# Performance work log

Hardware: AMD Instinct MI355X
Metric: run time of the kernel (lower is better)

## Reference

```python
import jax, jax.numpy as jnp
import numpy as np

# dims per init_kwargs / input_specs
B, S, HID = 4, 2048, 1024
H = 16          # num_heads
DH = HID // H   # head_dim = 64
G = 1024        # group_size; grouped feature dim = S*DH//G = 128
SCALE = 1.0 / (DH ** 0.5)


def setup_inputs() -> dict:
    key = jax.random.key(0)
    ks = jax.random.split(key, 9)
    w = lambda k: jax.random.normal(k, (HID, HID), jnp.float32) * 0.02
    b = lambda k: jax.random.normal(k, (HID,), jnp.float32) * 0.02
    return {
        "hidden_states": jax.random.normal(ks[0], (B, S, HID), jnp.float32),
        "Wq": w(ks[1]), "bq": b(ks[2]),
        "Wk": w(ks[3]), "bk": b(ks[4]),
        "Wv": w(ks[5]), "bv": b(ks[6]),
        "Wo": w(ks[7]), "bo": b(ks[8]),
    }


def reference(hidden_states, Wq, bq, Wk, bk, Wv, bv, Wo, bo):
    Bs, Ss, _ = hidden_states.shape

    def proj(W, bias):
        # torch nn.Linear: x @ W.T + b
        y = hidden_states @ W.T + bias                      # [B,S,HID]
        y = y.reshape(Bs, Ss, H, DH).transpose(0, 2, 1, 3)  # [B,H,S,DH]
        # grouped view: fold seq/head_dim into G groups of S*DH//G features
        return y.reshape(Bs, H, G, -1)                      # [B,H,G,S*DH/G]

    q, k, v = proj(Wq, bq), proj(Wk, bk), proj(Wv, bv)
    scores = jnp.einsum("bhgd,bhkd->bhgk", q, k) * SCALE    # [B,H,G,G]
    probs = jax.nn.softmax(scores, axis=-1)                 # dropout: eval mode (identity)
    ctx = jnp.einsum("bhgk,bhkd->bhgd", probs, v)           # [B,H,G,S*DH/G]
    ctx = ctx.transpose(0, 2, 1, 3).reshape(Bs, -1, HID)    # [B,S,HID]
    return ctx @ Wo.T + bo
```

## Files before the change

### kernel.cpp

```cpp
#include <hip/hip_runtime.h>


typedef __attribute__((ext_vector_type(8))) short short8;
typedef __attribute__((ext_vector_type(4))) float f32x4;
typedef unsigned int u32;
typedef unsigned short u16;

#define MFMA16(a, b, c) __builtin_amdgcn_mfma_f32_16x16x32_bf16((a), (b), (c), 0, 0, 0)

union S8 { short8 s; uint2 v[2]; u32 u[4]; };

__device__ __forceinline__ u32 f2bf1(float x) {
    union { float f; u32 u; } v; v.f = x;
    return (v.u + 0x7fffu + ((v.u >> 16) & 1u)) >> 16;
}

__device__ __forceinline__ u32 cvtpk(float lo, float hi) {
    u32 r;
    asm("v_cvt_pk_bf16_f32 %0, %1, %2" : "=v"(r) : "v"(lo), "v"(hi));
    return r;
}

__device__ __forceinline__ void gld16(u16* lds, const u16* g) {
    __builtin_amdgcn_global_load_lds(
        (const __attribute__((address_space(1))) unsigned int*)(g),
        (__attribute__((address_space(3))) unsigned int*)(lds),
        16, 0, 0);
}

__global__ __launch_bounds__(256) void convert(
    const float* __restrict__ X, const float* __restrict__ Wq,
    const float* __restrict__ Wk, const float* __restrict__ Wv,
    const float* __restrict__ Wo,
    u16* __restrict__ Xb, u16* __restrict__ Wcat, u16* __restrict__ Wob)
{
    const size_t M8 = 8388608, M1 = 1048576;
    size_t i = ((size_t)blockIdx.x * 256 + threadIdx.x) * 16;
    const float* src; u16* dst;
    if (i < M8)              { src = X  + i;                dst = Xb   + i; }
    else if (i < M8 + M1)    { src = Wq + (i - M8);         dst = Wcat + (i - M8); }
    else if (i < M8 + 2*M1)  { src = Wk + (i - M8 - M1);    dst = Wcat + (i - M8); }
    else if (i < M8 + 3*M1)  { src = Wv + (i - M8 - 2*M1);  dst = Wcat + (i - M8); }
    else                     { src = Wo + (i - M8 - 3*M1);  dst = Wob  + (i - M8 - 3*M1); }
#pragma unroll
    for (int j = 0; j < 2; ++j) {
        float4 a = ((const float4*)src)[2 * j];
        float4 b = ((const float4*)src)[2 * j + 1];
        uint4 o;
        o.x = f2bf1(a.x) | (f2bf1(a.y) << 16);
        o.y = f2bf1(a.z) | (f2bf1(a.w) << 16);
        o.z = f2bf1(b.x) | (f2bf1(b.y) << 16);
        o.w = f2bf1(b.z) | (f2bf1(b.w) << 16);
        ((uint4*)dst)[j] = o;
    }
}

__global__ __launch_bounds__(256, 2) void qkv_gemm10(
    const u16* __restrict__ Xb, const u16* __restrict__ Wcat,
    const float* __restrict__ b0, const float* __restrict__ b1,
    const float* __restrict__ b2,
    u16* __restrict__ q_att, u16* __restrict__ k_att, u16* __restrict__ v_t)
{
    const int nb = blockIdx.x, mb = blockIdx.y;
    const int mat = nb >> 3;

    __shared__ __align__(16) u16 As[2][128 * 64];
    __shared__ __align__(16) u16 Bs[2][128 * 64];

    const int t = threadIdx.x, wave = t >> 6, lane = t & 63;
    const int l15 = lane & 15, quad = lane >> 4;
    const int wm = (wave >> 1) * 64, wn = (wave & 1) * 64;

    const int srow = t >> 3;
    const int scol = ((t & 7) ^ (srow & 7)) * 8;

    const u16* Ab = Xb   + (size_t)(mb * 128) * 1024;
    const u16* Bb = Wcat + (size_t)(nb * 128) * 1024;

    const int swz = l15 & 7;

#define QSTAGE(pp, k0_) do {                                                  \
        _Pragma("unroll")                                                     \
        for (int c_ = 0; c_ < 4; ++c_) {                                      \
            size_t so_ = (size_t)(c_ * 32 + srow) * 1024 + (k0_) + scol;      \
            gld16(&As[(pp)][wave * 512 + c_ * 2048], Ab + so_);               \
            gld16(&Bs[(pp)][wave * 512 + c_ * 2048], Bb + so_);               \
        }                                                                     \
    } while (0)

    f32x4 acc[4][4] = {};

    QSTAGE(0, 0);
    __syncthreads();

    for (int kt = 0; kt < 16; ++kt) {
        const int p = kt & 1;
        if (kt + 1 < 16) QSTAGE(p ^ 1, (kt + 1) * 64);
        const u16* Asp = &As[p][0];
        const u16* Bsp = &Bs[p][0];

#pragma unroll
        for (int ks = 0; ks < 2; ++ks) {
            short8 af[4], bf[4];
            const int ck = ((ks * 4 + quad) ^ swz) * 8;
#pragma unroll
            for (int mt = 0; mt < 4; ++mt)
                af[mt] = *(const short8*)(Asp + (wm + mt * 16 + l15) * 64 + ck);
#pragma unroll
            for (int nt = 0; nt < 4; ++nt)
                bf[nt] = *(const short8*)(Bsp + (wn + nt * 16 + l15) * 64 + ck);
#pragma unroll
            for (int mt = 0; mt < 4; ++mt)
#pragma unroll
                for (int nt = 0; nt < 4; ++nt)
                    acc[mt][nt] = MFMA16(af[mt], bf[nt], acc[mt][nt]);
        }

        if (kt + 1 < 16) __syncthreads();
    }
#undef QSTAGE

    const float* bias = (mat == 0) ? b0 : (mat == 1) ? b1 : b2;
    const float scl = (mat == 0) ? 0.125f : 1.0f;
#pragma unroll
    for (int nt = 0; nt < 4; ++nt) {
        int colm = (nb & 7) * 128 + wn + nt * 16 + l15;
        float bv = bias[colm];
        int h = colm >> 6, dh = colm & 63;
#pragma unroll
        for (int mt = 0; mt < 4; ++mt) {
            int row0 = mb * 128 + wm + mt * 16 + quad * 4;
            int b = row0 >> 11, s0 = row0 & 2047;
            int bh = b * 16 + h, g0 = s0 >> 1;
            float v0 = (acc[mt][nt][0] + bv) * scl, v1 = (acc[mt][nt][1] + bv) * scl;
            float v2 = (acc[mt][nt][2] + bv) * scl, v3 = (acc[mt][nt][3] + bv) * scl;
            if (mat == 2) {
                u32 w0 = f2bf1(v0) | (f2bf1(v2) << 16);
                u32 w1 = f2bf1(v1) | (f2bf1(v3) << 16);
                int j6 = g0 & 63;
                int gp = (g0 & ~63) + (j6 & 32) + ((j6 >> 2) & 3) * 8
                       + ((j6 >> 4) & 1) * 4 + (j6 & 3);
                *(u32*)(v_t + ((size_t)(bh * 128 + dh) * 1024 + gp)) = w0;
                *(u32*)(v_t + ((size_t)(bh * 128 + dh + 64) * 1024 + gp)) = w1;
            } else {
                u16* dst = (mat == 0) ? q_att : k_att;
                u32 w0 = f2bf1(v0) | (f2bf1(v1) << 16);
                u32 w1 = f2bf1(v2) | (f2bf1(v3) << 16);
                size_t base = ((size_t)bh * 1024 + g0) * 128 + 2 * dh;
                *(u32*)(dst + base) = w0;
                *(u32*)(dst + base + 128) = w1;
            }
        }
    }
}

__global__ __launch_bounds__(256, 2) void attn5(
    const u16* __restrict__ q_att, const u16* __restrict__ k_att,
    const u16* __restrict__ v_t, u16* __restrict__ ctx)
{
    const int bh = blockIdx.x, qb = blockIdx.y;
    const u16* Q = q_att + (size_t)bh * 131072;
    const u16* K = k_att + (size_t)bh * 131072;
    const u16* V = v_t  + (size_t)bh * 131072;

    __shared__ __align__(16) u16 Ks[2][64 * 128];
    __shared__ __align__(16) u16 Vs[2][128 * 64];

    const int t = threadIdx.x, wave = t >> 6, lane = t & 63;
    const int l15 = lane & 15, quad = lane >> 4;

    int offK[4], offV[4];
#pragma unroll
    for (int j = 0; j < 4; ++j) {
        int ck = wave * 4 + j;
        int rowK = ck * 4 + (lane >> 4);
        offK[j] = rowK * 128 + (((lane & 15) ^ (rowK & 15)) * 8);
        int rowV = ck * 8 + (lane >> 3);
        offV[j] = rowV * 1024 + (((lane & 7) ^ ((lane >> 3) & 7)) * 8);
    }

#define ASTAGE(pp, kt) do {                                                   \
        const u16* Kt_ = K + (size_t)(kt) * 8192;                             \
        const u16* Vt_ = V + (size_t)(kt) * 64;                               \
        _Pragma("unroll")                                                     \
        for (int j_ = 0; j_ < 4; ++j_) {                                      \
            gld16(&Ks[(pp)][(wave * 4 + j_) * 512], Kt_ + offK[j_]);          \
            gld16(&Vs[(pp)][(wave * 4 + j_) * 512], Vt_ + offV[j_]);          \
        }                                                                     \
    } while (0)

    short8 bq[2][4];
#pragma unroll
    for (int qg = 0; qg < 2; ++qg) {
        const int qr = qb * 128 + wave * 32 + qg * 16 + l15;
#pragma unroll
        for (int kb = 0; kb < 4; ++kb)
            bq[qg][kb] = *(const short8*)(Q + (size_t)qr * 128 + kb * 32 + quad * 8);
    }

    f32x4 accO[2][8] = {};
    float m_i[2] = {-1e30f, -1e30f}, l_i[2] = {0.0f, 0.0f};

    ASTAGE(0, 0);
    __syncthreads();

    for (int kt = 0; kt < 16; ++kt) {
        const int p = kt & 1;
        if (kt + 1 < 16) ASTAGE(p ^ 1, kt + 1);
        const u16* Ksp = &Ks[p][0];
        const u16* Vsp = &Vs[p][0];

        f32x4 accS[2][4] = {};
        __builtin_amdgcn_s_setprio(1);
#pragma unroll
        for (int kf = 0; kf < 4; ++kf)
#pragma unroll
            for (int kb = 0; kb < 4; ++kb) {
                short8 ak = *(const short8*)(Ksp + (kf * 16 + l15) * 128
                                             + (((kb * 4 + quad) ^ l15) * 8));
                accS[0][kf] = MFMA16(ak, bq[0][kb], accS[0][kf]);
                accS[1][kf] = MFMA16(ak, bq[1][kb], accS[1][kf]);
            }
        __builtin_amdgcn_s_setprio(0);

        u32 pb[2][8];
#pragma unroll
        for (int qg = 0; qg < 2; ++qg) {
            float mloc = -1e30f;
#pragma unroll
            for (int kf = 0; kf < 4; ++kf)
                mloc = fmaxf(mloc, fmaxf(fmaxf(accS[qg][kf][0], accS[qg][kf][1]),
                                         fmaxf(accS[qg][kf][2], accS[qg][kf][3])));
            mloc = fmaxf(mloc, __shfl_xor(mloc, 16));
            mloc = fmaxf(mloc, __shfl_xor(mloc, 32));

            if (!__all(mloc - m_i[qg] <= 8.0f)) {
                float mn = fmaxf(m_i[qg], mloc);
                float alpha = __expf(m_i[qg] - mn);
#pragma unroll
                for (int f = 0; f < 8; ++f) {
                    accO[qg][f][0] *= alpha; accO[qg][f][1] *= alpha;
                    accO[qg][f][2] *= alpha; accO[qg][f][3] *= alpha;
                }
                l_i[qg] *= alpha;
                m_i[qg] = mn;
            }

            float lsum = 0.0f;
            const float mi = m_i[qg];
#pragma unroll
            for (int kf = 0; kf < 4; ++kf) {
                float p0 = __expf(accS[qg][kf][0] - mi);
                float p1 = __expf(accS[qg][kf][1] - mi);
                float p2 = __expf(accS[qg][kf][2] - mi);
                float p3 = __expf(accS[qg][kf][3] - mi);
                lsum += (p0 + p1) + (p2 + p3);
                pb[qg][kf * 2]     = cvtpk(p0, p1);
                pb[qg][kf * 2 + 1] = cvtpk(p2, p3);
            }
            lsum += __shfl_xor(lsum, 16);
            lsum += __shfl_xor(lsum, 32);
            l_i[qg] += lsum;
        }

        S8 bp00, bp01, bp10, bp11;
        bp00.u[0] = pb[0][0]; bp00.u[1] = pb[0][1]; bp00.u[2] = pb[0][2]; bp00.u[3] = pb[0][3];
        bp01.u[0] = pb[0][4]; bp01.u[1] = pb[0][5]; bp01.u[2] = pb[0][6]; bp01.u[3] = pb[0][7];
        bp10.u[0] = pb[1][0]; bp10.u[1] = pb[1][1]; bp10.u[2] = pb[1][2]; bp10.u[3] = pb[1][3];
        bp11.u[0] = pb[1][4]; bp11.u[1] = pb[1][5]; bp11.u[2] = pb[1][6]; bp11.u[3] = pb[1][7];
        const int l7 = l15 & 7;
        __builtin_amdgcn_s_setprio(1);
#pragma unroll
        for (int df = 0; df < 8; ++df) {
            const u16* vrow = Vsp + (df * 16 + l15) * 64;
            short8 av0 = *(const short8*)(vrow + ((quad ^ l7) * 8));
            short8 av1 = *(const short8*)(vrow + (((quad + 4) ^ l7) * 8));
            accO[0][df] = MFMA16(av0, bp00.s, accO[0][df]);
            accO[0][df] = MFMA16(av1, bp01.s, accO[0][df]);
            accO[1][df] = MFMA16(av0, bp10.s, accO[1][df]);
            accO[1][df] = MFMA16(av1, bp11.s, accO[1][df]);
        }
        __builtin_amdgcn_s_setprio(0);

        if (kt + 1 < 16) __syncthreads();
    }
#undef ASTAGE

    const int h = bh & 15, b = bh >> 4;
#pragma unroll
    for (int qg = 0; qg < 2; ++qg) {
        const int qr = qb * 128 + wave * 32 + qg * 16 + l15;
        float inv = 1.0f / l_i[qg];
        size_t base = ((size_t)(b * 2048 + 2 * qr + (h >> 3))) * 1024 + (h & 7) * 128;
#pragma unroll
        for (int df = 0; df < 8; ++df) {
            int dp = df * 16 + quad * 4;
            uint2 w;
            w.x = f2bf1(accO[qg][df][0] * inv) | (f2bf1(accO[qg][df][1] * inv) << 16);
            w.y = f2bf1(accO[qg][df][2] * inv) | (f2bf1(accO[qg][df][3] * inv) << 16);
            *(uint2*)(ctx + base + dp) = w;
        }
    }
}

__global__ __launch_bounds__(256, 2) void out_gemm10(
    const u16* __restrict__ ctx, const u16* __restrict__ Wob,
    const float* __restrict__ bo, float* __restrict__ out)
{
    const int nb = blockIdx.x, mb = blockIdx.y;
    __shared__ __align__(16) u16 As[2][128 * 64];
    __shared__ __align__(16) u16 Bs[2][128 * 64];
    const int t = threadIdx.x, wave = t >> 6, lane = t & 63;
    const int l15 = lane & 15, quad = lane >> 4;
    const int wm = (wave >> 1) * 64, wn = (wave & 1) * 64;

    const int srow = t >> 3;
    const int scol = ((t & 7) ^ (srow & 7)) * 8;

    const u16* Ab = ctx + (size_t)(mb * 128) * 1024;
    const u16* Bb = Wob + (size_t)(nb * 128) * 1024;

    const int swz = l15 & 7;

#define OSTAGE(pp, k0_) do {                                                  \
        _Pragma("unroll")                                                     \
        for (int c_ = 0; c_ < 4; ++c_) {                                      \
            size_t so_ = (size_t)(c_ * 32 + srow) * 1024 + (k0_) + scol;      \
            gld16(&As[(pp)][wave * 512 + c_ * 2048], Ab + so_);               \
            gld16(&Bs[(pp)][wave * 512 + c_ * 2048], Bb + so_);               \
        }                                                                     \
    } while (0)

    f32x4 acc[4][4] = {};

    OSTAGE(0, 0);
    __syncthreads();

    for (int kt = 0; kt < 16; ++kt) {
        const int p = kt & 1;
        if (kt + 1 < 16) OSTAGE(p ^ 1, (kt + 1) * 64);
        const u16* Asp = &As[p][0];
        const u16* Bsp = &Bs[p][0];

#pragma unroll
        for (int ks = 0; ks < 2; ++ks) {
            short8 af[4], bf[4];
            const int ck = ((ks * 4 + quad) ^ swz) * 8;
#pragma unroll
            for (int mt = 0; mt < 4; ++mt)
                af[mt] = *(const short8*)(Asp + (wm + mt * 16 + l15) * 64 + ck);
#pragma unroll
            for (int nt = 0; nt < 4; ++nt)
                bf[nt] = *(const short8*)(Bsp + (wn + nt * 16 + l15) * 64 + ck);
#pragma unroll
            for (int mt = 0; mt < 4; ++mt)
#pragma unroll
                for (int nt = 0; nt < 4; ++nt)
                    acc[mt][nt] = MFMA16(af[mt], bf[nt], acc[mt][nt]);
        }

        if (kt + 1 < 16) __syncthreads();
    }
#undef OSTAGE

#pragma unroll
    for (int nt = 0; nt < 4; ++nt) {
        int col = nb * 128 + wn + nt * 16 + l15;
        float bv = bo[col];
#pragma unroll
        for (int mt = 0; mt < 4; ++mt)
#pragma unroll
            for (int r = 0; r < 4; ++r) {
                int row = mb * 128 + wm + mt * 16 + quad * 4 + r;
                out[(size_t)row * 1024 + col] = acc[mt][nt][r] + bv;
            }
    }
}

extern "C" void kernel_launch(void* const* d_in, const int* in_sizes, int n_in,
                              void* d_out, int out_size, void* d_ws, size_t ws_size,
                              hipStream_t stream)
{
    const float* X  = (const float*)d_in[0];
    const float* Wq = (const float*)d_in[1];
    const float* bq = (const float*)d_in[2];
    const float* Wk = (const float*)d_in[3];
    const float* bk = (const float*)d_in[4];
    const float* Wv = (const float*)d_in[5];
    const float* bv = (const float*)d_in[6];
    const float* Wo = (const float*)d_in[7];
    const float* bo = (const float*)d_in[8];

    const size_t M8 = 8388608;
    u16* q_att = (u16*)d_ws;
    u16* k_att = q_att + M8;
    u16* v_t   = k_att + M8;
    u16* Xb    = v_t   + M8;
    u16* ctx   = Xb;
    u16* Wcat  = Xb + M8;
    u16* Wob   = Wcat + 3 * 1048576;

    convert<<<dim3(3072), 256, 0, stream>>>(X, Wq, Wk, Wv, Wo, Xb, Wcat, Wob);
    qkv_gemm10<<<dim3(24, 64), 256, 0, stream>>>(Xb, Wcat, bq, bk, bv,
                                                 q_att, k_att, v_t);
    attn5<<<dim3(64, 8), 256, 0, stream>>>(q_att, k_att, v_t, ctx);
    out_gemm10<<<dim3(8, 64), 256, 0, stream>>>(ctx, Wob, bo, (float*)d_out);
}
```

Baseline: 242.0 us.

## Single-buffer QKV GEMM LDS and prefetch after fragment loads for higher occupancy

The QKV projection GEMM drops its double-buffered LDS tiles to one buffer, halving shared memory so three blocks can fit per CU (launch bounds raised to 3). Each k-step first reads all A/B fragments for both sub-steps into registers, then syncs and issues the next tile's global-to-LDS loads, and runs the MFMAs while those loads are in flight. This trades the double-buffer overlap for more resident blocks, at the cost of more fragment registers and an extra barrier per iteration.

```diff
diff --git a/kernel.cpp b/kernel.cpp
--- a/kernel.cpp
+++ b/kernel.cpp
@@ -55,7 +55,7 @@
     }
 }
 
-__global__ __launch_bounds__(256, 2) void qkv_gemm10(
+__global__ __launch_bounds__(256, 3) void qkv_gemm11(
     const u16* __restrict__ Xb, const u16* __restrict__ Wcat,
     const float* __restrict__ b0, const float* __restrict__ b1,
     const float* __restrict__ b2,
@@ -64,8 +64,8 @@
     const int nb = blockIdx.x, mb = blockIdx.y;
     const int mat = nb >> 3;
 
-    __shared__ __align__(16) u16 As[2][128 * 64];
-    __shared__ __align__(16) u16 Bs[2][128 * 64];
+    __shared__ __align__(16) u16 As[128 * 64];
+    __shared__ __align__(16) u16 Bs[128 * 64];
 
     const int t = threadIdx.x, wave = t >> 6, lane = t & 63;
     const int l15 = lane & 15, quad = lane >> 4;
@@ -79,42 +79,46 @@
 
     const int swz = l15 & 7;
 
-#define QSTAGE(pp, k0_) do {                                                  \
+#define QSTAGE(k0_) do {                                                      \
         _Pragma("unroll")                                                     \
         for (int c_ = 0; c_ < 4; ++c_) {                                      \
             size_t so_ = (size_t)(c_ * 32 + srow) * 1024 + (k0_) + scol;      \
-            gld16(&As[(pp)][wave * 512 + c_ * 2048], Ab + so_);               \
-            gld16(&Bs[(pp)][wave * 512 + c_ * 2048], Bb + so_);               \
+            gld16(As + wave * 512 + c_ * 2048, Ab + so_);                     \
+            gld16(Bs + wave * 512 + c_ * 2048, Bb + so_);                     \
         }                                                                     \
     } while (0)
 
     f32x4 acc[4][4] = {};
 
-    QSTAGE(0, 0);
+    QSTAGE(0);
     __syncthreads();
 
     for (int kt = 0; kt < 16; ++kt) {
-        const int p = kt & 1;
-        if (kt + 1 < 16) QSTAGE(p ^ 1, (kt + 1) * 64);
-        const u16* Asp = &As[p][0];
-        const u16* Bsp = &Bs[p][0];
-
+        short8 af[4][2], bf[4][2];
 #pragma unroll
         for (int ks = 0; ks < 2; ++ks) {
-            short8 af[4], bf[4];
             const int ck = ((ks * 4 + quad) ^ swz) * 8;
 #pragma unroll
             for (int mt = 0; mt < 4; ++mt)
-                af[mt] = *(const short8*)(Asp + (wm + mt * 16 + l15) * 64 + ck);
+                af[mt][ks] = *(const short8*)(As + (wm + mt * 16 + l15) * 64 + ck);
 #pragma unroll
             for (int nt = 0; nt < 4; ++nt)
-                bf[nt] = *(const short8*)(Bsp + (wn + nt * 16 + l15) * 64 + ck);
+                bf[nt][ks] = *(const short8*)(Bs + (wn + nt * 16 + l15) * 64 + ck);
+        }
+
+        if (kt + 1 < 16) {
+            __syncthreads();
+            QSTAGE((kt + 1) * 64);
+        }
+        __builtin_amdgcn_sched_barrier(0);
+
+#pragma unroll
+        for (int ks = 0; ks < 2; ++ks)
 #pragma unroll
             for (int mt = 0; mt < 4; ++mt)
 #pragma unroll
                 for (int nt = 0; nt < 4; ++nt)
-                    acc[mt][nt] = MFMA16(af[mt], bf[nt], acc[mt][nt]);
-        }
+                    acc[mt][nt] = MFMA16(af[mt][ks], bf[nt][ks], acc[mt][nt]);
 
         if (kt + 1 < 16) __syncthreads();
     }
@@ -401,7 +405,7 @@
     u16* Wob   = Wcat + 3 * 1048576;
 
     convert<<<dim3(3072), 256, 0, stream>>>(X, Wq, Wk, Wv, Wo, Xb, Wcat, Wob);
-    qkv_gemm10<<<dim3(24, 64), 256, 0, stream>>>(Xb, Wcat, bq, bk, bv,
+    qkv_gemm11<<<dim3(24, 64), 256, 0, stream>>>(Xb, Wcat, bq, bk, bv,
                                                  q_att, k_att, v_t);
     attn5<<<dim3(64, 8), 256, 0, stream>>>(q_att, k_att, v_t, ctx);
     out_gemm10<<<dim3(8, 64), 256, 0, stream>>>(ctx, Wob, bo, (float*)d_out);
```

New measurement: 238.8 us. Within noise of the previous version (-1.3%).
